# Kernel tuning notes

Measured on AMD Instinct MI355X. Metric: run time of the kernel, lower is better.

Reference implementation:

```python
import jax, jax.numpy as jnp
import numpy as np

N_HEAD = 16
ROPE_BASE = 10000.0


def rotate_half(x):
    d = x.shape[-1] // 2
    return jnp.concatenate((-x[..., d:], x[..., :d]), axis=-1)


def rope_cos_sin(T, head_dim, dtype):
    inv_freq = 1.0 / (ROPE_BASE ** (jnp.arange(0, head_dim, 2, dtype=jnp.float32) / head_dim))
    t = jnp.arange(T, dtype=jnp.float32)
    freqs = jnp.einsum('i,j->ij', t, inv_freq)  # [T, head_dim/2]
    emb = jnp.concatenate((freqs, freqs), axis=-1)  # [T, head_dim]
    return jnp.cos(emb).astype(dtype), jnp.sin(emb).astype(dtype)


def setup_inputs() -> dict:
    key = jax.random.key(0)
    k1, k2, k3 = jax.random.split(key, 3)
    B, T, C = 4, 2048, 2048
    x = jax.random.normal(k1, (B, T, C), dtype=jnp.float32)
    w_attn = jax.random.normal(k2, (3 * C, C), dtype=jnp.float32) * (1.0 / np.sqrt(C))
    w_proj = jax.random.normal(k3, (C, C), dtype=jnp.float32) * (1.0 / np.sqrt(C))
    return {"x": x, "w_attn": w_attn, "w_proj": w_proj}


def reference(x, w_attn, w_proj):
    B, T, C = x.shape
    H = N_HEAD
    D = C // H
    qkv = jnp.einsum('btc,fc->btf', x, w_attn)  # [B, T, 3C]
    q, k, v = jnp.split(qkv, 3, axis=-1)
    # [B, H, T, D]
    q = q.reshape(B, T, H, D).transpose(0, 2, 1, 3)
    k = k.reshape(B, T, H, D).transpose(0, 2, 1, 3)
    v = v.reshape(B, T, H, D).transpose(0, 2, 1, 3)
    cos, sin = rope_cos_sin(T, D, x.dtype)  # [T, D]
    cos = cos[None, None, :, :]
    sin = sin[None, None, :, :]
    q = q * cos + rotate_half(q) * sin
    k = k * cos + rotate_half(k) * sin
    # bidirectional SDPA
    scale = 1.0 / jnp.sqrt(jnp.asarray(D, dtype=x.dtype))
    att = jnp.einsum('bhtd,bhsd->bhts', q, k) * scale
    att = jax.nn.softmax(att, axis=-1)
    y = jnp.einsum('bhts,bhsd->bhtd', att, v)
    y = y.transpose(0, 2, 1, 3).reshape(B, T, C)
    return jnp.einsum('btc,oc->bto', y, w_proj)
```

## Files before the change

### kernel.cpp

```cpp
#include <hip/hip_runtime.h>

#define DEVINL __device__ __forceinline__

typedef unsigned short u16;
typedef __attribute__((ext_vector_type(8))) __bf16 bf16x8;
typedef __attribute__((ext_vector_type(4))) float f32x4;
typedef __attribute__((ext_vector_type(16))) float f32x16;

struct alignas(8) u16x4 { u16 x, y, z, w; };

#define MFMA16(a, b, c) __builtin_amdgcn_mfma_f32_16x16x32_bf16(a, b, c, 0, 0, 0)
#define MFMA32(a, b, c) __builtin_amdgcn_mfma_f32_32x32x16_bf16(a, b, c, 0, 0, 0)

DEVINL u16 f2bf(float f) {
  unsigned u = __builtin_bit_cast(unsigned, f);
  u += 0x7fffu + ((u >> 16) & 1u);
  return (u16)(u >> 16);
}

DEVINL unsigned cvtpk_bf16(float lo, float hi) {
  unsigned r;
  asm("v_cvt_pk_bf16_f32 %0, %1, %2" : "=v"(r) : "v"(lo), "v"(hi));
  return r;
}

DEVINL void plane_swap(unsigned& a, unsigned& b) {
  asm("v_permlane32_swap_b32 %0, %1" : "+v"(a), "+v"(b));
}

DEVINL void gload_lds16(const u16* g, u16* l) {
  __builtin_amdgcn_global_load_lds((const __attribute__((address_space(1))) void*)g,
                                   (__attribute__((address_space(3))) void*)l,
                                   16, 0, 0);
}

DEVINL bf16x8 frag64(const u16* lds, int row, int cg) {
  int c = cg ^ (row & 7);
  return *(const bf16x8*)(lds + row * 64 + c * 8);
}
DEVINL bf16x8 frag128(const u16* lds, int row, int cg) {
  int c = cg ^ (row & 7);
  return *(const bf16x8*)(lds + row * 128 + c * 8);
}

DEVINL void stage_k512(const u16* g, u16* lds, int wave, int lane) {
#pragma unroll
  for (int t = 0; t < 2; ++t) {
    int r = t * 32 + wave * 4 + (lane >> 4);
    int cg = (lane & 15) ^ (r & 7);
    gload_lds16(g + (size_t)r * 128 + cg * 8, lds + (t * 32 + wave * 4) * 128);
  }
}
DEVINL void stage_v512(const u16* g, int ldg, u16* lds, int wave, int lane) {
#pragma unroll
  for (int t = 0; t < 2; ++t) {
    int r = t * 64 + wave * 8 + (lane >> 3);
    int cg = (lane & 7) ^ (r & 7);
    gload_lds16(g + (size_t)r * ldg + cg * 8, lds + (t * 64 + wave * 8) * 64);
  }
}

DEVINL int perm32(int row) { return (row & 3) ^ ((row >> 2) & 3); }

DEVINL void stage32(const u16* g, int ldg, u16* lds, int q, int wave, int lane) {
  int row = q * 128 + wave * 16 + (lane >> 2);
  int cg = (lane & 3) ^ perm32(row);
  gload_lds16(g + (size_t)row * ldg + cg * 8, lds + (q * 128 + wave * 16) * 32);
}

DEVINL bf16x8 frag32(const u16* lds, int row, int lc) {
  int c = lc ^ perm32(row);
  return *(const bf16x8*)(lds + row * 32 + c * 8);
}

__global__ void __launch_bounds__(256) k_cast(const float* __restrict__ src,
                                              u16* __restrict__ dst, int n4) {
  int i = blockIdx.x * blockDim.x + threadIdx.x;
  int stride = gridDim.x * blockDim.x;
  for (; i < n4; i += stride) {
    float4 f = ((const float4*)src)[i];
    u16x4 u;
    u.x = f2bf(f.x); u.y = f2bf(f.y); u.z = f2bf(f.z); u.w = f2bf(f.w);
    ((u16x4*)dst)[i] = u;
  }
}

DEVINL void gemm_loop256(const u16* Ag, const u16* Bg, int K, u16* smem,
                         f32x4 acc[8][4], int wave, int lane) {
  const int wm = wave >> 2, wn = wave & 3;
  const int lr = lane & 15, lc = lane >> 4;

#pragma unroll
  for (int t = 0; t < 3; ++t) {
    u16* At = smem + t * 8192;
    u16* Bt = smem + 32768 + t * 8192;
    stage32(Ag + t * 32, K, At, 0, wave, lane);
    stage32(Ag + t * 32, K, At, 1, wave, lane);
    stage32(Bg + t * 32, K, Bt, 0, wave, lane);
    stage32(Bg + t * 32, K, Bt, 1, wave, lane);
  }

  const int nsteps = K / 32;
  for (int s = 0; s < nsteps; ++s) {
    const int slot = s & 3;
    if (s + 2 < nsteps) {
      asm volatile("s_waitcnt vmcnt(8)" ::: "memory");
    } else if (s + 1 < nsteps) {
      asm volatile("s_waitcnt vmcnt(4)" ::: "memory");
    } else {
      asm volatile("s_waitcnt vmcnt(0)" ::: "memory");
    }
    asm volatile("s_barrier" ::: "memory");

    const u16* Ac = smem + slot * 8192;
    const u16* Bc = smem + 32768 + slot * 8192;
    const bool do_stage = (s + 3 < nsteps);
    u16* An = smem + ((s + 3) & 3) * 8192;
    u16* Bn = smem + 32768 + ((s + 3) & 3) * 8192;
    const u16* Agn = Ag + (size_t)(s + 3) * 32;
    const u16* Bgn = Bg + (size_t)(s + 3) * 32;

    __builtin_amdgcn_s_setprio(1);
    bf16x8 bfr[4];
#pragma unroll
    for (int nf = 0; nf < 4; ++nf)
      bfr[nf] = frag32(Bc, nf * 64 + wn * 16 + lr, lc);
    bf16x8 aA[4];
#pragma unroll
    for (int mf = 0; mf < 4; ++mf)
      aA[mf] = frag32(Ac, wm * 128 + mf * 16 + lr, lc);
    if (do_stage) {
      stage32(Agn, K, An, 0, wave, lane);
      stage32(Agn, K, An, 1, wave, lane);
    }
#pragma unroll
    for (int mf = 0; mf < 4; ++mf)
#pragma unroll
      for (int nf = 0; nf < 4; ++nf)
        acc[mf][nf] = MFMA16(aA[mf], bfr[nf], acc[mf][nf]);
    __builtin_amdgcn_s_setprio(0);
    asm volatile("s_barrier" ::: "memory");

    __builtin_amdgcn_s_setprio(1);
    bf16x8 aB[4];
#pragma unroll
    for (int mf = 0; mf < 4; ++mf)
      aB[mf] = frag32(Ac, wm * 128 + (mf + 4) * 16 + lr, lc);
    if (do_stage) {
      stage32(Bgn, K, Bn, 0, wave, lane);
      stage32(Bgn, K, Bn, 1, wave, lane);
    }
#pragma unroll
    for (int mf = 0; mf < 4; ++mf)
#pragma unroll
      for (int nf = 0; nf < 4; ++nf)
        acc[mf + 4][nf] = MFMA16(aB[mf], bfr[nf], acc[mf + 4][nf]);
    __builtin_amdgcn_s_setprio(0);
    asm volatile("s_barrier" ::: "memory");
  }
}

__global__ void __launch_bounds__(512, 2) k_gemm_qkv(const u16* __restrict__ xb,
                                                     const u16* __restrict__ wab,
                                                     u16* __restrict__ qb,
                                                     u16* __restrict__ kb,
                                                     u16* __restrict__ vtb) {
  extern __shared__ u16 smem[];
  int bid = blockIdx.x;
  int sw = (bid & 7) * 96 + (bid >> 3);
  const int tm = sw / 24, tn = sw % 24;
  const int wave = threadIdx.x >> 6, lane = threadIdx.x & 63;
  const int wm = wave >> 2, wn = wave & 3;
  const int lr = lane & 15, lc = lane >> 4;

  f32x4 acc[8][4];
#pragma unroll
  for (int i = 0; i < 8; ++i)
#pragma unroll
    for (int n = 0; n < 4; ++n) acc[i][n] = f32x4{0.f, 0.f, 0.f, 0.f};

  gemm_loop256(xb + (size_t)tm * 256 * 2048, wab + (size_t)tn * 256 * 2048, 2048,
               smem, acc, wave, lane);

  const int sel = tn >> 3;
  const int hh = (tn & 7) * 2;
  const int m0 = tm * 256 + wm * 128;
  const int b = (tm * 256) >> 11;

  if (sel < 2) {
    u16* dst = sel ? kb : qb;
    const float qs = sel ? 1.0f : 0.12751745f;
    const int d = wn * 16 + lr;
    const float invf = __expf(-0.14391156631f * (float)d);
#pragma unroll
    for (int mf = 0; mf < 8; ++mf) {
#pragma unroll
      for (int j = 0; j < 4; ++j) {
        int t = (m0 + mf * 16 + lc * 4 + j) & 2047;
        float ang = (float)t * invf;
        float s, c;
        __sincosf(ang, &s, &c);
#pragma unroll
        for (int hp = 0; hp < 2; ++hp) {
          float lo = acc[mf][2 * hp][j];
          float hi = acc[mf][2 * hp + 1][j];
          size_t rowp = ((size_t)(b * 16 + hh + hp) * 2048 + t) * 128;
          dst[rowp + d] = f2bf((lo * c - hi * s) * qs);
          dst[rowp + d + 64] = f2bf((hi * c + lo * s) * qs);
        }
      }
    }
  } else {
#pragma unroll
    for (int mf = 0; mf < 8; ++mf) {
      int t0 = (m0 + mf * 16 + lc * 4) & 2047;
#pragma unroll
      for (int nf = 0; nf < 4; ++nf) {
        int d = wn * 16 + lr + (nf & 1) * 64;
        int h = hh + (nf >> 1);
        u16x4 pk;
        pk.x = f2bf(acc[mf][nf][0]);
        pk.y = f2bf(acc[mf][nf][1]);
        pk.z = f2bf(acc[mf][nf][2]);
        pk.w = f2bf(acc[mf][nf][3]);
        *(u16x4*)(vtb + ((size_t)(b * 16 + h) * 128 + d) * 2048 + t0) = pk;
      }
    }
  }
}

__global__ void __launch_bounds__(512, 2) k_gemm_proj(const u16* __restrict__ yb,
                                                      const u16* __restrict__ wpb,
                                                      float* __restrict__ out) {
  extern __shared__ u16 smem[];
  int bid = blockIdx.x;
  int sw = (bid & 7) * 32 + (bid >> 3);
  const int tm = sw >> 3, tn = sw & 7;
  const int wave = threadIdx.x >> 6, lane = threadIdx.x & 63;
  const int wm = wave >> 2, wn = wave & 3;
  const int lr = lane & 15, lc = lane >> 4;

  f32x4 acc[8][4];
#pragma unroll
  for (int i = 0; i < 8; ++i)
#pragma unroll
    for (int n = 0; n < 4; ++n) acc[i][n] = f32x4{0.f, 0.f, 0.f, 0.f};

  gemm_loop256(yb + (size_t)tm * 256 * 2048, wpb + (size_t)tn * 256 * 2048, 2048,
               smem, acc, wave, lane);

  const int m0 = tm * 256 + wm * 128;
#pragma unroll
  for (int mf = 0; mf < 8; ++mf) {
#pragma unroll
    for (int j = 0; j < 4; ++j) {
      int gr = m0 + mf * 16 + lc * 4 + j;
      float* op = out + (size_t)gr * 2048 + tn * 256 + wn * 16 + lr;
#pragma unroll
      for (int nf = 0; nf < 4; ++nf) op[nf * 64] = acc[mf][nf][j];
    }
  }
}

__global__ void __launch_bounds__(512) k_attn(const u16* __restrict__ qg,
                                              const u16* __restrict__ kg,
                                              const u16* __restrict__ vtg,
                                              u16* __restrict__ yg) {
  __shared__ u16 Ks[2][64 * 128];
  __shared__ u16 Vs[2][128 * 64];
  int bid = blockIdx.x;
  int sw = (bid & 7) * 64 + (bid >> 3);
  const int qt = sw & 7, bh = sw >> 3;
  const int wave = threadIdx.x >> 6, lane = threadIdx.x & 63;
  const int hi = lane >> 5, ln = lane & 31;

  const u16* qbh = qg + (size_t)bh * (2048 * 128);
  const u16* kbh = kg + (size_t)bh * (2048 * 128);
  const u16* vbh = vtg + (size_t)bh * (128 * 2048);
  const int qrow0 = qt * 256 + wave * 32;

  bf16x8 qf[8];
#pragma unroll
  for (int kc = 0; kc < 8; ++kc)
    qf[kc] = *(const bf16x8*)(qbh + (size_t)(qrow0 + ln) * 128 + kc * 16 + hi * 8);

  f32x16 yacc[4];
#pragma unroll
  for (int nd = 0; nd < 4; ++nd)
#pragma unroll
    for (int r = 0; r < 16; ++r) yacc[nd][r] = 0.f;
  float m = -1e30f, l = 0.f;

  stage_k512(kbh, Ks[0], wave, lane);
  stage_v512(vbh, 2048, Vs[0], wave, lane);
  __syncthreads();

  int buf = 0;
  for (int kv0 = 0; kv0 < 2048; kv0 += 64) {
    if (kv0 + 64 < 2048) {
      stage_k512(kbh + (size_t)(kv0 + 64) * 128, Ks[buf ^ 1], wave, lane);
      stage_v512(vbh + kv0 + 64, 2048, Vs[buf ^ 1], wave, lane);
    }
    const u16* Kb = Ks[buf];
    const u16* Vb = Vs[buf];

    f32x16 st[2];
#pragma unroll
    for (int h2 = 0; h2 < 2; ++h2)
#pragma unroll
      for (int r = 0; r < 16; ++r) st[h2][r] = 0.f;
    __builtin_amdgcn_s_setprio(1);
#pragma unroll
    for (int kc = 0; kc < 8; ++kc) {
      bf16x8 a0 = frag128(Kb, ln, kc * 2 + hi);
      bf16x8 a1 = frag128(Kb, 32 + ln, kc * 2 + hi);
      st[0] = MFMA32(a0, qf[kc], st[0]);
      st[1] = MFMA32(a1, qf[kc], st[1]);
    }
    __builtin_amdgcn_s_setprio(0);

    float t8[8];
#pragma unroll
    for (int i = 0; i < 8; ++i)
      t8[i] = fmaxf(fmaxf(st[0][i], st[0][i + 8]), fmaxf(st[1][i], st[1][i + 8]));
    float pmax = fmaxf(fmaxf(fmaxf(t8[0], t8[4]), fmaxf(t8[1], t8[5])),
                       fmaxf(fmaxf(t8[2], t8[6]), fmaxf(t8[3], t8[7])));
    pmax = fmaxf(pmax, __shfl_xor(pmax, 32));

    if (__any(pmax - m > 11.5415603f)) {
      float mn = fmaxf(m, pmax);
      float al = __builtin_amdgcn_exp2f(m - mn);
      m = mn;
      l *= al;
#pragma unroll
      for (int nd = 0; nd < 4; ++nd)
#pragma unroll
        for (int r = 0; r < 16; ++r) yacc[nd][r] *= al;
    }

    float sa0 = 0.f, sa1 = 0.f, sa2 = 0.f, sa3 = 0.f;
#pragma unroll
    for (int h2 = 0; h2 < 2; ++h2) {
#pragma unroll
      for (int r = 0; r < 16; ++r) {
        float e = __builtin_amdgcn_exp2f(st[h2][r] - m);
        st[h2][r] = e;
        if ((r & 3) == 0) sa0 += e;
        else if ((r & 3) == 1) sa1 += e;
        else if ((r & 3) == 2) sa2 += e;
        else sa3 += e;
      }
    }
    float ssum = (sa0 + sa1) + (sa2 + sa3);
    ssum += __shfl_xor(ssum, 32);
    l += ssum;

    unsigned wa[2][4], wb[2][4];
#pragma unroll
    for (int h2 = 0; h2 < 2; ++h2)
#pragma unroll
      for (int q8 = 0; q8 < 4; ++q8) {
        wa[h2][q8] = cvtpk_bf16(st[h2][q8 * 4 + 0], st[h2][q8 * 4 + 1]);
        wb[h2][q8] = cvtpk_bf16(st[h2][q8 * 4 + 2], st[h2][q8 * 4 + 3]);
      }

    __builtin_amdgcn_s_setprio(1);
#pragma unroll
    for (int ks = 0; ks < 4; ++ks) {
      const int h2 = ks >> 1, k1 = ks & 1;
      unsigned w0 = wa[h2][2 * k1], w2 = wa[h2][2 * k1 + 1];
      plane_swap(w0, w2);
      unsigned w1 = wb[h2][2 * k1], w3 = wb[h2][2 * k1 + 1];
      plane_swap(w1, w3);
      union { unsigned u[4]; bf16x8 v; } pa;
      pa.u[0] = w0; pa.u[1] = w1; pa.u[2] = w2; pa.u[3] = w3;
#pragma unroll
      for (int nd = 0; nd < 4; ++nd) {
        bf16x8 bv = frag64(Vb, nd * 32 + ln, 2 * ks + hi);
        yacc[nd] = MFMA32(pa.v, bv, yacc[nd]);
      }
    }
    __builtin_amdgcn_s_setprio(0);

    __syncthreads();
    buf ^= 1;
  }

  const int b = bh >> 4, h = bh & 15;
  float inv = 1.f / l;
#pragma unroll
  for (int r = 0; r < 16; ++r) {
    int crow = (r & 3) + 8 * (r >> 2) + 4 * hi;
    float li = __shfl(inv, crow);
    int t = qrow0 + crow;
    size_t rp = ((size_t)b * 2048 + t) * 2048 + h * 128;
#pragma unroll
    for (int nd = 0; nd < 4; ++nd)
      yg[rp + nd * 32 + ln] = f2bf(yacc[nd][r] * li);
  }
}

extern "C" void kernel_launch(void* const* d_in, const int* in_sizes, int n_in,
                              void* d_out, int out_size, void* d_ws, size_t ws_size,
                              hipStream_t stream) {
  const float* x = (const float*)d_in[0];
  const float* wa = (const float*)d_in[1];
  const float* wp = (const float*)d_in[2];
  float* out = (float*)d_out;

  u16* xb = (u16*)d_ws;
  u16* wab = xb + 16777216;
  u16* wpb = wab + 12582912;
  u16* qb = wpb + 4194304;
  u16* kb = qb + 16777216;
  u16* vtb = kb + 16777216;
  u16* yb = vtb + 16777216;

  hipFuncSetAttribute((const void*)k_gemm_qkv,
                      hipFuncAttributeMaxDynamicSharedMemorySize, 131072);
  hipFuncSetAttribute((const void*)k_gemm_proj,
                      hipFuncAttributeMaxDynamicSharedMemorySize, 131072);

  k_cast<<<dim3(2048), dim3(256), 0, stream>>>(x, xb, 4194304);
  k_cast<<<dim3(2048), dim3(256), 0, stream>>>(wa, wab, 3145728);
  k_cast<<<dim3(1024), dim3(256), 0, stream>>>(wp, wpb, 1048576);
  k_gemm_qkv<<<dim3(768), dim3(512), 131072, stream>>>(xb, wab, qb, kb, vtb);
  k_attn<<<dim3(512), dim3(512), 0, stream>>>(qb, kb, vtb, yb);
  k_gemm_proj<<<dim3(256), dim3(512), 131072, stream>>>(yb, wpb, out);
}
```

Baseline: 464.4 us.

## Fuse cast kernels, restructure GEMM barriers, and remap QKV tiles per XCD

The three fp32-to-bf16 cast launches become a single kernel that picks its source and destination buffers by block index. The GEMM main loop moves its vmcnt wait and barrier to the end of each step and puts a barrier before each MFMA phase, so LDS reads and the next global stage are issued before waiting. The QKV GEMM block-to-tile mapping changes so each XCD works on a contiguous 8x12 region of tiles, which is meant to improve L2 reuse. The barrier reordering risks subtle LDS hazards if the wait counts are off.

```diff
diff --git a/kernel.cpp b/kernel.cpp
--- a/kernel.cpp
+++ b/kernel.cpp
@@ -73,15 +73,31 @@
   return *(const bf16x8*)(lds + row * 32 + c * 8);
 }
 
-__global__ void __launch_bounds__(256) k_cast(const float* __restrict__ src,
-                                              u16* __restrict__ dst, int n4) {
-  int i = blockIdx.x * blockDim.x + threadIdx.x;
-  int stride = gridDim.x * blockDim.x;
-  for (; i < n4; i += stride) {
-    float4 f = ((const float4*)src)[i];
+__global__ void __launch_bounds__(256) k_cast3(const float4* __restrict__ x,
+                                               const float4* __restrict__ wa,
+                                               const float4* __restrict__ wp,
+                                               u16x4* __restrict__ xb,
+                                               u16x4* __restrict__ wab,
+                                               u16x4* __restrict__ wpb) {
+  const int b = blockIdx.x;
+  const float4* src;
+  u16x4* dst;
+  int n, i, stride;
+  if (b < 1024) {
+    src = x; dst = xb; n = 4194304;
+    i = b * 256 + threadIdx.x; stride = 1024 * 256;
+  } else if (b < 1792) {
+    src = wa; dst = wab; n = 3145728;
+    i = (b - 1024) * 256 + threadIdx.x; stride = 768 * 256;
+  } else {
+    src = wp; dst = wpb; n = 1048576;
+    i = (b - 1792) * 256 + threadIdx.x; stride = 256 * 256;
+  }
+  for (; i < n; i += stride) {
+    float4 f = src[i];
     u16x4 u;
     u.x = f2bf(f.x); u.y = f2bf(f.y); u.z = f2bf(f.z); u.w = f2bf(f.w);
-    ((u16x4*)dst)[i] = u;
+    dst[i] = u;
   }
 }
 
@@ -99,19 +115,12 @@
     stage32(Bg + t * 32, K, Bt, 0, wave, lane);
     stage32(Bg + t * 32, K, Bt, 1, wave, lane);
   }
+  asm volatile("s_waitcnt vmcnt(8)" ::: "memory");
+  asm volatile("s_barrier" ::: "memory");
 
   const int nsteps = K / 32;
   for (int s = 0; s < nsteps; ++s) {
     const int slot = s & 3;
-    if (s + 2 < nsteps) {
-      asm volatile("s_waitcnt vmcnt(8)" ::: "memory");
-    } else if (s + 1 < nsteps) {
-      asm volatile("s_waitcnt vmcnt(4)" ::: "memory");
-    } else {
-      asm volatile("s_waitcnt vmcnt(0)" ::: "memory");
-    }
-    asm volatile("s_barrier" ::: "memory");
-
     const u16* Ac = smem + slot * 8192;
     const u16* Bc = smem + 32768 + slot * 8192;
     const bool do_stage = (s + 3 < nsteps);
@@ -120,12 +129,10 @@
     const u16* Agn = Ag + (size_t)(s + 3) * 32;
     const u16* Bgn = Bg + (size_t)(s + 3) * 32;
 
-    __builtin_amdgcn_s_setprio(1);
-    bf16x8 bfr[4];
+    bf16x8 bfr[4], aA[4];
 #pragma unroll
     for (int nf = 0; nf < 4; ++nf)
       bfr[nf] = frag32(Bc, nf * 64 + wn * 16 + lr, lc);
-    bf16x8 aA[4];
 #pragma unroll
     for (int mf = 0; mf < 4; ++mf)
       aA[mf] = frag32(Ac, wm * 128 + mf * 16 + lr, lc);
@@ -133,15 +140,15 @@
       stage32(Agn, K, An, 0, wave, lane);
       stage32(Agn, K, An, 1, wave, lane);
     }
+    asm volatile("s_barrier" ::: "memory");
+    __builtin_amdgcn_s_setprio(1);
 #pragma unroll
     for (int mf = 0; mf < 4; ++mf)
 #pragma unroll
       for (int nf = 0; nf < 4; ++nf)
         acc[mf][nf] = MFMA16(aA[mf], bfr[nf], acc[mf][nf]);
     __builtin_amdgcn_s_setprio(0);
-    asm volatile("s_barrier" ::: "memory");
-
-    __builtin_amdgcn_s_setprio(1);
+
     bf16x8 aB[4];
 #pragma unroll
     for (int mf = 0; mf < 4; ++mf)
@@ -150,13 +157,24 @@
       stage32(Bgn, K, Bn, 0, wave, lane);
       stage32(Bgn, K, Bn, 1, wave, lane);
     }
+    asm volatile("s_barrier" ::: "memory");
+    __builtin_amdgcn_s_setprio(1);
 #pragma unroll
     for (int mf = 0; mf < 4; ++mf)
 #pragma unroll
       for (int nf = 0; nf < 4; ++nf)
         acc[mf + 4][nf] = MFMA16(aB[mf], bfr[nf], acc[mf + 4][nf]);
     __builtin_amdgcn_s_setprio(0);
-    asm volatile("s_barrier" ::: "memory");
+
+    if (s + 3 < nsteps) {
+      asm volatile("s_waitcnt vmcnt(8)" ::: "memory");
+    } else if (s + 2 < nsteps) {
+      asm volatile("s_waitcnt vmcnt(4)" ::: "memory");
+    } else if (s + 1 < nsteps) {
+      asm volatile("s_waitcnt vmcnt(0)" ::: "memory");
+    }
+    if (s + 1 < nsteps)
+      asm volatile("s_barrier" ::: "memory");
   }
 }
 
@@ -167,8 +185,9 @@
                                                      u16* __restrict__ vtb) {
   extern __shared__ u16 smem[];
   int bid = blockIdx.x;
-  int sw = (bid & 7) * 96 + (bid >> 3);
-  const int tm = sw / 24, tn = sw % 24;
+  const int xcd = bid & 7, local = bid >> 3;
+  const int tm = (xcd & 3) * 8 + (local & 7);
+  const int tn = (xcd >> 2) * 12 + (local >> 3);
   const int wave = threadIdx.x >> 6, lane = threadIdx.x & 63;
   const int wm = wave >> 2, wn = wave & 3;
   const int lr = lane & 15, lc = lane >> 4;
@@ -421,9 +440,9 @@
   hipFuncSetAttribute((const void*)k_gemm_proj,
                       hipFuncAttributeMaxDynamicSharedMemorySize, 131072);
 
-  k_cast<<<dim3(2048), dim3(256), 0, stream>>>(x, xb, 4194304);
-  k_cast<<<dim3(2048), dim3(256), 0, stream>>>(wa, wab, 3145728);
-  k_cast<<<dim3(1024), dim3(256), 0, stream>>>(wp, wpb, 1048576);
+  k_cast3<<<dim3(2048), dim3(256), 0, stream>>>(
+      (const float4*)x, (const float4*)wa, (const float4*)wp,
+      (u16x4*)xb, (u16x4*)wab, (u16x4*)wpb);
   k_gemm_qkv<<<dim3(768), dim3(512), 131072, stream>>>(xb, wab, qb, kb, vtb);
   k_attn<<<dim3(512), dim3(512), 0, stream>>>(qb, kb, vtb, yb);
   k_gemm_proj<<<dim3(256), dim3(512), 131072, stream>>>(yb, wpb, out);
```

Measured after the change: 463.8 us. Within noise of the previous version (-0.1%).
